# Performance work log

Hardware: AMD Instinct MI355X
Metric: run time of the kernel (lower is better)

Reference implementation:

```python
import jax, jax.numpy as jnp
import numpy as np

D_MODEL = 1024
D_INNER = 1024          # expand=1
NQK = 32
NV = 32
DSTATE = 64
DCONV = 4
CHUNK = 128
CONV_DIM = D_INNER + 2 * NQK * DSTATE          # 5120
HEADDIM = D_INNER // NV                         # 32
IN_PROJ_OUT = 2 * D_INNER + 2 * NQK * DSTATE + NV  # 6176


def setup_inputs() -> dict:
    key = jax.random.key(0)
    ks = jax.random.split(key, 6)
    B, L = 2, 8192
    u = jax.random.normal(ks[0], (B, L, D_MODEL), jnp.float32)
    W_in = jax.random.normal(ks[1], (IN_PROJ_OUT, D_MODEL), jnp.float32) * 0.02
    conv_w = jax.random.normal(ks[2], (CONV_DIM, DCONV), jnp.float32) * 0.2
    conv_b = jax.random.normal(ks[3], (CONV_DIM,), jnp.float32) * 0.02
    z_bias = jnp.zeros((D_INNER,), jnp.float32)
    D = jnp.ones((NV,), jnp.float32)
    W_out = jax.random.normal(ks[4], (D_MODEL, D_INNER), jnp.float32) * 0.02
    return {"u": u, "W_in": W_in, "conv_w": conv_w, "conv_b": conv_b,
            "z_bias": z_bias, "D": D, "W_out": W_out}


def _segsum(x):
    # x: (b,h,c,l) -> (b,h,c,l,l); entry (i,j) = sum_{j<s<=i} x_s for i>=j, masked else
    l = x.shape[-1]
    cs = jnp.cumsum(x, -1)
    seg = cs[..., :, None] - cs[..., None, :]
    mask = jnp.tril(jnp.ones((l, l), bool))
    return jnp.where(mask, seg, -1e9)


def reference(u, W_in, conv_w, conv_b, z_bias, D, W_out):
    b, L, _ = u.shape
    # in_proj and split: xBC | z | A_log
    xBCzA = u @ W_in.T
    xBC = xBCzA[..., :CONV_DIM]
    z = xBCzA[..., CONV_DIM:CONV_DIM + D_INNER]
    A_log = xBCzA[..., CONV_DIM + D_INNER:]          # (b,L,NV)
    # causal depthwise conv1d, identity activation
    xp = jnp.pad(xBC, ((0, 0), (DCONV - 1, 0), (0, 0)))
    xBC = sum(conv_w[:, k] * xp[:, k:k + L, :] for k in range(DCONV)) + conv_b
    # split x, B, C and reshape to heads
    x = xBC[..., :D_INNER].reshape(b, L, NV, HEADDIM)
    Bm = xBC[..., D_INNER:D_INNER + NQK * DSTATE].reshape(b, L, NQK, DSTATE)
    Cm = xBC[..., D_INNER + NQK * DSTATE:].reshape(b, L, NQK, DSTATE)
    # dt = softplus(A_log); A = -1 per head; kernel uses (x/dt) and multiplies dt back in
    dt = jax.nn.softplus(A_log)                      # (b,L,h)
    x_sc = x / dt[..., None]
    Xdt = x_sc * dt[..., None]
    Adt = -dt
    # chunked SSD (mamba_chunk_scan_combined math)
    nc = L // CHUNK
    Ac = Adt.reshape(b, nc, CHUNK, NV).transpose(0, 3, 1, 2)   # (b,h,c,l)
    A_cum = jnp.cumsum(Ac, -1)
    Lmat = jnp.exp(_segsum(Ac))                                # (b,h,c,l,l)
    Bc = Bm.reshape(b, nc, CHUNK, NQK, DSTATE)
    Cc = Cm.reshape(b, nc, CHUNK, NQK, DSTATE)
    Xc = Xdt.reshape(b, nc, CHUNK, NV, HEADDIM)
    # intra-chunk (diagonal block) output
    Y_diag = jnp.einsum('bclhn,bcshn,bhcls,bcshp->bclhp', Cc, Bc, Lmat, Xc)
    # per-chunk final states
    decay_states = jnp.exp(A_cum[..., -1:] - A_cum)            # (b,h,c,l)
    states = jnp.einsum('bclhn,bhcl,bclhp->bchpn', Bc, decay_states, Xc)
    dc = jnp.exp(A_cum[..., -1])                               # (b,h,c)
    st = jnp.moveaxis(states, 1, 0)                            # (c,b,h,p,n)
    dcs = jnp.moveaxis(dc, 2, 0)                               # (c,b,h)

    def step(S, inp):
        s_c, d_c = inp
        prev = S
        S = S * d_c[..., None, None] + s_c
        return S, prev

    S0 = jnp.zeros((b, NV, HEADDIM, DSTATE), Xdt.dtype)
    _, prevs = jax.lax.scan(step, S0, (st, dcs))               # (c,b,h,p,n)
    prevs = jnp.moveaxis(prevs, 0, 1)                          # (b,c,h,p,n)
    # inter-chunk (off-diagonal) contribution
    Y_off = jnp.einsum('bclhn,bchpn,bhcl->bclhp', Cc, prevs, jnp.exp(A_cum))
    y = (Y_diag + Y_off).reshape(b, L, NV, HEADDIM)
    # skip connection uses the UNscaled x (per torch code)
    y = y + D[None, None, :, None] * x
    y = y.reshape(b, L, D_INNER)
    # gated output projection
    return (y * jax.nn.silu(z + z_bias)) @ W_out.T
```

## Files before the change

kernel.cpp:

```cpp
#include <hip/hip_runtime.h>

typedef unsigned short u16;
typedef unsigned int   u32;
typedef __bf16  bf16x8 __attribute__((ext_vector_type(8)));
typedef float   f32x4  __attribute__((ext_vector_type(4)));
typedef unsigned int u32x4 __attribute__((ext_vector_type(4)));
typedef unsigned int u32x2 __attribute__((ext_vector_type(2)));

__device__ __forceinline__ float bf2f(u16 h){ return __uint_as_float(((u32)h)<<16); }
__device__ __forceinline__ u16 f2bf(float f){
  u32 u = __float_as_uint(f);
  u += 0x7FFFu + ((u>>16)&1u);
  return (u16)(u>>16);
}
__device__ __forceinline__ f32x4 mfma16(bf16x8 a, bf16x8 b, f32x4 c){
  return __builtin_amdgcn_mfma_f32_16x16x32_bf16(a,b,c,0,0,0);
}

__global__ __launch_bounds__(256) void cvt_kernel(const float* __restrict__ in,
                                                  u16* __restrict__ out, int n4){
  int i = blockIdx.x*256 + threadIdx.x;
  if (i < n4){
    float4 v = ((const float4*)in)[i];
    u32 p0 = (u32)f2bf(v.x) | ((u32)f2bf(v.y)<<16);
    u32 p1 = (u32)f2bf(v.z) | ((u32)f2bf(v.w)<<16);
    u32x2 pv = {p0, p1};
    *(u32x2*)(out + (size_t)i*4) = pv;
  }
}

__global__ __launch_bounds__(256) void dt_kernel(const float* __restrict__ u,
                                                 const float* __restrict__ Win,
                                                 float* __restrict__ dtb){
  __shared__ float us[8][1028];
  const int tid = threadIdx.x;
  const size_t t0 = (size_t)blockIdx.x*8;
  for (int i=tid; i<2048; i+=256){
    int row = i>>8, col = (i&255)*4;
    *(float4*)&us[row][col] = *(const float4*)(u + (t0+row)*1024 + col);
  }
  __syncthreads();
  const int tok = tid & 7, h = tid >> 3;
  const float* wp = Win + (size_t)(6144+h)*1024;
  float s0=0.f,s1=0.f,s2=0.f,s3=0.f;
  for (int k=0;k<1024;k+=4){
    float4 a  = *(const float4*)&us[tok][k];
    float4 wv = *(const float4*)&wp[k];
    s0 += a.x*wv.x; s1 += a.y*wv.y; s2 += a.z*wv.z; s3 += a.w*wv.w;
  }
  float s = (s0+s1)+(s2+s3);
  dtb[(t0+tok)*32 + h] = (s > 15.f) ? s : log1pf(expf(s));
}

__global__ __launch_bounds__(256,2) void gemm_in(const float* __restrict__ A,
                                                 const u16* __restrict__ Bw,
                                                 u16* __restrict__ out0,
                                                 u16* __restrict__ out1,
                                                 const float* __restrict__ zb){
  __shared__ u16 As[128*40];
  __shared__ u16 Bs[128*40];
  const int tid  = threadIdx.x;
  const int lane = tid & 63;
  const int w = tid >> 6, wm = w >> 1, wn = w & 1;
  const int quad = lane >> 4, l15 = lane & 15;
  const size_t m0 = (size_t)blockIdx.y*128, n0 = (size_t)blockIdx.x*128;

  f32x4 acc[4][4];
  #pragma unroll
  for (int i=0;i<4;i++)
    #pragma unroll
    for (int j=0;j<4;j++){ f32x4 z = {0.f,0.f,0.f,0.f}; acc[i][j] = z; }

  const int srow = tid >> 2;
  const int scol = (tid & 3) * 8;

  for (int k0 = 0; k0 < 1024; k0 += 32){
    __syncthreads();
    #pragma unroll
    for (int p=0;p<2;p++){
      int row = srow + p*64;
      const float* ap = A + (m0+row)*1024 + k0 + scol;
      float4 a0 = *(const float4*)ap;
      float4 a1 = *(const float4*)(ap+4);
      u32 w0 = (u32)f2bf(a0.x) | ((u32)f2bf(a0.y)<<16);
      u32 w1 = (u32)f2bf(a0.z) | ((u32)f2bf(a0.w)<<16);
      u32 w2 = (u32)f2bf(a1.x) | ((u32)f2bf(a1.y)<<16);
      u32 w3 = (u32)f2bf(a1.z) | ((u32)f2bf(a1.w)<<16);
      u32x4 va = {w0,w1,w2,w3};
      *(u32x4*)&As[row*40 + scol] = va;
      u32x4 vb = *(const u32x4*)(Bw + (n0+row)*1024 + k0 + scol);
      *(u32x4*)&Bs[row*40 + scol] = vb;
    }
    __syncthreads();
    bf16x8 av[4], bv[4];
    #pragma unroll
    for (int mi=0;mi<4;mi++) av[mi] = *(const bf16x8*)&As[(wm*64+mi*16+l15)*40 + quad*8];
    #pragma unroll
    for (int ni=0;ni<4;ni++) bv[ni] = *(const bf16x8*)&Bs[(wn*64+ni*16+l15)*40 + quad*8];
    #pragma unroll
    for (int mi=0;mi<4;mi++)
      #pragma unroll
      for (int ni=0;ni<4;ni++)
        acc[mi][ni] = mfma16(av[mi], bv[ni], acc[mi][ni]);
  }

  #pragma unroll
  for (int mi=0;mi<4;mi++){
    #pragma unroll
    for (int ni=0;ni<4;ni++){
      #pragma unroll
      for (int r=0;r<4;r++){
        size_t row = m0 + wm*64 + mi*16 + quad*4 + r;
        int    col = (int)n0 + wn*64 + ni*16 + l15;
        float v = acc[mi][ni][r];
        if (col < 5120){
          out0[row*5120 + col] = f2bf(v);
        } else {
          int ch = col - 5120;
          float z = v + zb[ch];
          float sg = z / (1.f + __expf(-z));
          out1[row*1024 + ch] = f2bf(sg);
        }
      }
    }
  }
}

__global__ __launch_bounds__(256,2) void gemm_out(const u16* __restrict__ A,
                                                  const u16* __restrict__ Bw,
                                                  float* __restrict__ out0){
  __shared__ u16 As[128*40];
  __shared__ u16 Bs[128*40];
  const int tid  = threadIdx.x;
  const int lane = tid & 63;
  const int w = tid >> 6, wm = w >> 1, wn = w & 1;
  const int quad = lane >> 4, l15 = lane & 15;
  const size_t m0 = (size_t)blockIdx.y*128, n0 = (size_t)blockIdx.x*128;

  f32x4 acc[4][4];
  #pragma unroll
  for (int i=0;i<4;i++)
    #pragma unroll
    for (int j=0;j<4;j++){ f32x4 z = {0.f,0.f,0.f,0.f}; acc[i][j] = z; }

  const int srow = tid >> 2;
  const int scol = (tid & 3) * 8;

  for (int k0 = 0; k0 < 1024; k0 += 32){
    __syncthreads();
    #pragma unroll
    for (int p=0;p<2;p++){
      int row = srow + p*64;
      u32x4 va = *(const u32x4*)(A  + (m0+row)*1024 + k0 + scol);
      u32x4 vb = *(const u32x4*)(Bw + (n0+row)*1024 + k0 + scol);
      *(u32x4*)&As[row*40 + scol] = va;
      *(u32x4*)&Bs[row*40 + scol] = vb;
    }
    __syncthreads();
    bf16x8 av[4], bv[4];
    #pragma unroll
    for (int mi=0;mi<4;mi++) av[mi] = *(const bf16x8*)&As[(wm*64+mi*16+l15)*40 + quad*8];
    #pragma unroll
    for (int ni=0;ni<4;ni++) bv[ni] = *(const bf16x8*)&Bs[(wn*64+ni*16+l15)*40 + quad*8];
    #pragma unroll
    for (int mi=0;mi<4;mi++)
      #pragma unroll
      for (int ni=0;ni<4;ni++)
        acc[mi][ni] = mfma16(av[mi], bv[ni], acc[mi][ni]);
  }

  #pragma unroll
  for (int mi=0;mi<4;mi++)
    #pragma unroll
    for (int ni=0;ni<4;ni++)
      #pragma unroll
      for (int r=0;r<4;r++){
        size_t row = m0 + wm*64 + mi*16 + quad*4 + r;
        int    col = (int)n0 + wn*64 + ni*16 + l15;
        out0[row*1024 + col] = acc[mi][ni][r];
      }
}

__global__ __launch_bounds__(256) void conv_kernel(const u16* __restrict__ xraw,
                                                   const float* __restrict__ cw,
                                                   const float* __restrict__ cb,
                                                   u16* __restrict__ xconv){
  const int c  = blockIdx.x*256 + threadIdx.x;
  const int t0 = blockIdx.y*8;
  const float w0=cw[c*4+0], w1=cw[c*4+1], w2=cw[c*4+2], w3=cw[c*4+3], bias=cb[c];
  const size_t base = (size_t)c;
  float h0 = (t0>=3) ? bf2f(xraw[base + (size_t)(t0-3)*5120]) : 0.f;
  float h1 = (t0>=2) ? bf2f(xraw[base + (size_t)(t0-2)*5120]) : 0.f;
  float h2 = (t0>=1) ? bf2f(xraw[base + (size_t)(t0-1)*5120]) : 0.f;
  #pragma unroll
  for (int i=0;i<8;i++){
    float x = bf2f(xraw[base + (size_t)(t0+i)*5120]);
    float o = w0*h0 + w1*h1 + w2*h2 + w3*x + bias;
    xconv[base + (size_t)(t0+i)*5120] = f2bf(o);
    h0=h1; h1=h2; h2=x;
  }
}

__global__ __launch_bounds__(256,1) void chunk1_kernel(const u16* __restrict__ xconv,
                                                       const float* __restrict__ dtb,
                                                       const float* __restrict__ Dvec,
                                                       float* __restrict__ ypart,
                                                       float* __restrict__ states,
                                                       float* __restrict__ dcb){
  __shared__ u16 Ps[128*136];
  __shared__ u16 XT[32*136];
  __shared__ u16 BT[64*136];
  __shared__ float Acum[128];
  __shared__ float decay[128];

  const int tid = threadIdx.x;
  const int lane = tid & 63;
  const int w = tid >> 6, quad = lane >> 4, l15 = lane & 15;
  const int blk = blockIdx.x;
  const int h = blk & 31, c = blk >> 5;
  const size_t tok0 = (size_t)c*128;
  const size_t xbase = tok0 * 5120;

  float mdt = 0.f;
  if (tid < 128) mdt = -dtb[(tok0 + tid)*32 + h];

  #pragma unroll
  for (int p=0;p<2;p++){
    int idx = p*256 + tid;
    int row = idx >> 2, col = (idx & 3)*8;
    u32x4 v = *(const u32x4*)(xconv + xbase + (size_t)row*5120 + h*32 + col);
    const u16* pv = (const u16*)&v;
    #pragma unroll
    for (int j=0;j<8;j++) XT[(col+j)*136 + row] = pv[j];
  }
  #pragma unroll
  for (int p=0;p<4;p++){
    int idx = p*256 + tid;
    int row = idx >> 3, col = (idx & 7)*8;
    u32x4 v = *(const u32x4*)(xconv + xbase + (size_t)row*5120 + 1024 + h*64 + col);
    const u16* pv = (const u16*)&v;
    #pragma unroll
    for (int j=0;j<8;j++) BT[(col+j)*136 + row] = pv[j];
  }
  if (tid < 128) Acum[tid] = mdt;
  __syncthreads();
  float run = mdt;
  for (int off=1; off<128; off<<=1){
    float add = 0.f;
    if (tid < 128 && tid >= off) add = Acum[tid-off];
    __syncthreads();
    if (tid < 128){ run += add; Acum[tid] = run; }
    __syncthreads();
  }
  float Alast = Acum[127];
  if (tid < 128) decay[tid] = __expf(Alast - Acum[tid]);
  if (tid == 0)  dcb[blk] = __expf(Alast);

  const int wm = w >> 1, wn = w & 1;
  f32x4 g[4][4];
  #pragma unroll
  for (int i=0;i<4;i++)
    #pragma unroll
    for (int j=0;j<4;j++){ f32x4 z = {0.f,0.f,0.f,0.f}; g[i][j] = z; }
  #pragma unroll
  for (int kk=0; kk<2; kk++){
    bf16x8 av[4], bv[4];
    #pragma unroll
    for (int mi=0;mi<4;mi++){
      int row = wm*64 + mi*16 + l15;
      av[mi] = *(const bf16x8*)(xconv + xbase + (size_t)row*5120 + 3072 + h*64 + kk*32 + quad*8);
    }
    #pragma unroll
    for (int ni=0;ni<4;ni++){
      int row = wn*64 + ni*16 + l15;
      bv[ni] = *(const bf16x8*)(xconv + xbase + (size_t)row*5120 + 1024 + h*64 + kk*32 + quad*8);
    }
    #pragma unroll
    for (int mi=0;mi<4;mi++)
      #pragma unroll
      for (int ni=0;ni<4;ni++)
        g[mi][ni] = mfma16(av[mi], bv[ni], g[mi][ni]);
  }
  #pragma unroll
  for (int mi=0;mi<4;mi++){
    int rowb = wm*64 + mi*16 + quad*4;
    #pragma unroll
    for (int ni=0;ni<4;ni++){
      int col = wn*64 + ni*16 + l15;
      float ac = Acum[col];
      #pragma unroll
      for (int r=0;r<4;r++){
        int row = rowb + r;
        float val = 0.f;
        if (col <= row) val = g[mi][ni][r] * __expf(Acum[row] - ac);
        Ps[row*136 + col] = f2bf(val);
      }
    }
  }
  __syncthreads();

  f32x4 yd[2][2];
  #pragma unroll
  for (int i=0;i<2;i++)
    #pragma unroll
    for (int j=0;j<2;j++){ f32x4 z = {0.f,0.f,0.f,0.f}; yd[i][j] = z; }
  #pragma unroll
  for (int kk=0;kk<4;kk++){
    bf16x8 av[2], bv[2];
    #pragma unroll
    for (int mi=0;mi<2;mi++) av[mi] = *(const bf16x8*)&Ps[(w*32+mi*16+l15)*136 + kk*32 + quad*8];
    #pragma unroll
    for (int ni=0;ni<2;ni++) bv[ni] = *(const bf16x8*)&XT[(ni*16+l15)*136 + kk*32 + quad*8];
    #pragma unroll
    for (int mi=0;mi<2;mi++)
      #pragma unroll
      for (int ni=0;ni<2;ni++)
        yd[mi][ni] = mfma16(av[mi], bv[ni], yd[mi][ni]);
  }
  float Dh = Dvec[h];
  #pragma unroll
  for (int mi=0;mi<2;mi++)
    #pragma unroll
    for (int ni=0;ni<2;ni++)
      #pragma unroll
      for (int r=0;r<4;r++){
        int row = w*32 + mi*16 + quad*4 + r;
        int col = ni*16 + l15;
        float xval = bf2f(XT[col*136 + row]);
        ypart[(tok0+row)*1024 + h*32 + col] = yd[mi][ni][r] + Dh*xval;
      }

  const int wm2 = w >> 1, wn2 = w & 1;
  f32x4 st[2];
  { f32x4 z = {0.f,0.f,0.f,0.f}; st[0]=z; st[1]=z; }
  #pragma unroll
  for (int kk=0;kk<4;kk++){
    bf16x8 av;
    {
      u32x4 xv = *(const u32x4*)&XT[(wm2*16+l15)*136 + kk*32 + quad*8];
      const u16* xp = (const u16*)&xv;
      #pragma unroll
      for (int j=0;j<8;j++) ((__bf16*)&av)[j] = (__bf16)(bf2f(xp[j]) * decay[kk*32 + quad*8 + j]);
    }
    bf16x8 bv[2];
    #pragma unroll
    for (int ni=0;ni<2;ni++) bv[ni] = *(const bf16x8*)&BT[(wn2*32+ni*16+l15)*136 + kk*32 + quad*8];
    #pragma unroll
    for (int ni=0;ni<2;ni++) st[ni] = mfma16(av, bv[ni], st[ni]);
  }
  size_t sbase = (size_t)blk * 2048;
  #pragma unroll
  for (int ni=0;ni<2;ni++)
    #pragma unroll
    for (int r=0;r<4;r++){
      int row = wm2*16 + quad*4 + r;
      int col = wn2*32 + ni*16 + l15;
      states[sbase + row*64 + col] = st[ni][r];
    }
}

__global__ __launch_bounds__(256) void scan_kernel(float* __restrict__ states,
                                                   const float* __restrict__ dcb){
  const int h = blockIdx.x >> 3;
  const int part = blockIdx.x & 7;
  const int pn = part*256 + threadIdx.x;
  float S = 0.f;
  for (int c=0;c<64;c++){
    size_t idx = ((size_t)(c*32 + h))*2048 + pn;
    float stv = states[idx];
    float d = dcb[c*32 + h];
    states[idx] = S;
    S = S*d + stv;
  }
}

__global__ __launch_bounds__(256,1) void chunk3_kernel(const u16* __restrict__ xconv,
                                                       const float* __restrict__ dtb,
                                                       const float* __restrict__ prevs,
                                                       const float* __restrict__ ypart,
                                                       const u16* __restrict__ gate,
                                                       u16* __restrict__ yg){
  __shared__ u16 Pv[32*72];
  __shared__ float Acum[128];
  const int tid = threadIdx.x;
  const int lane = tid & 63;
  const int w = tid >> 6, quad = lane >> 4, l15 = lane & 15;
  const int blk = blockIdx.x;
  const int h = blk & 31, c = blk >> 5;
  const size_t tok0 = (size_t)c*128;
  const size_t xbase = tok0 * 5120;

  float mdt = 0.f;
  if (tid < 128) mdt = -dtb[(tok0 + tid)*32 + h];
  size_t sbase = (size_t)blk * 2048;
  #pragma unroll
  for (int p=0;p<8;p++){
    int i = p*256 + tid;
    int pp = i >> 6, nn = i & 63;
    Pv[pp*72 + nn] = f2bf(prevs[sbase + i]);
  }
  if (tid < 128) Acum[tid] = mdt;
  __syncthreads();
  float run = mdt;
  for (int off=1; off<128; off<<=1){
    float add = 0.f;
    if (tid < 128 && tid >= off) add = Acum[tid-off];
    __syncthreads();
    if (tid < 128){ run += add; Acum[tid] = run; }
    __syncthreads();
  }

  f32x4 yo[2][2];
  #pragma unroll
  for (int i=0;i<2;i++)
    #pragma unroll
    for (int j=0;j<2;j++){ f32x4 z = {0.f,0.f,0.f,0.f}; yo[i][j] = z; }
  #pragma unroll
  for (int kk=0;kk<2;kk++){
    bf16x8 av[2], bv[2];
    #pragma unroll
    for (int mi=0;mi<2;mi++){
      int row = w*32 + mi*16 + l15;
      av[mi] = *(const bf16x8*)(xconv + xbase + (size_t)row*5120 + 3072 + h*64 + kk*32 + quad*8);
    }
    #pragma unroll
    for (int ni=0;ni<2;ni++) bv[ni] = *(const bf16x8*)&Pv[(ni*16+l15)*72 + kk*32 + quad*8];
    #pragma unroll
    for (int mi=0;mi<2;mi++)
      #pragma unroll
      for (int ni=0;ni<2;ni++)
        yo[mi][ni] = mfma16(av[mi], bv[ni], yo[mi][ni]);
  }
  #pragma unroll
  for (int mi=0;mi<2;mi++)
    #pragma unroll
    for (int ni=0;ni<2;ni++)
      #pragma unroll
      for (int r=0;r<4;r++){
        int row = w*32 + mi*16 + quad*4 + r;
        int col = ni*16 + l15;
        size_t gi = (tok0+row)*1024 + h*32 + col;
        float val = (ypart[gi] + __expf(Acum[row]) * yo[mi][ni][r]) * bf2f(gate[gi]);
        yg[gi] = f2bf(val);
      }
}

extern "C" void kernel_launch(void* const* d_in, const int* in_sizes, int n_in,
                              void* d_out, int out_size, void* d_ws, size_t ws_size,
                              hipStream_t stream){
  (void)out_size; (void)ws_size;
  static const int want[7] = {16777216, 6324224, 20480, 5120, 1024, 32, 1048576};
  const void* src[7] = {nullptr,nullptr,nullptr,nullptr,nullptr,nullptr,nullptr};
  if (n_in >= 7){
    for (int i=0;i<7;i++)
      for (int j=0;j<n_in;j++)
        if (in_sizes[j] == want[i]){ src[i] = d_in[j]; break; }
  }
  bool ok = true;
  for (int i=0;i<7;i++) if (!src[i]) ok = false;
  if (!ok) for (int i=0;i<7;i++) src[i] = d_in[i];
  const float* u      = (const float*)src[0];
  const float* W_in   = (const float*)src[1];
  const float* conv_w = (const float*)src[2];
  const float* conv_b = (const float*)src[3];
  const float* z_bias = (const float*)src[4];
  const float* Dvec   = (const float*)src[5];
  const float* W_out  = (const float*)src[6];
  float* out = (float*)d_out;

  char* p = (char*)d_ws;
  u16* wi_bf   = (u16*)p;   p += (size_t)6144*1024*2;
  u16* wo_bf   = (u16*)p;   p += (size_t)1024*1024*2;
  float* dtb   = (float*)p; p += (size_t)16384*32*4;
  u16* yg      = (u16*)p;   p += (size_t)16384*1024*2;
  float* dcb   = (float*)p; p += (size_t)4096*4;
  u16* gate    = (u16*)p;   p += (size_t)8192*1024*2;
  char* xbcA   = p;         p += (size_t)8192*5120*2;
  u16* xconv   = (u16*)p;   p += (size_t)8192*5120*2;

  u16*   xbc_raw = (u16*)xbcA;
  float* ypart   = (float*)xbcA;
  float* states  = (float*)(xbcA + (size_t)8192*1024*4);

  cvt_kernel<<<6144, 256, 0, stream>>>(W_in,  wi_bf, 6144*1024/4);
  cvt_kernel<<<1024, 256, 0, stream>>>(W_out, wo_bf, 1024*1024/4);
  dt_kernel<<<2048, 256, 0, stream>>>(u, W_in, dtb);

  for (int b = 0; b < 2; b++){
    const float* u_b   = u   + (size_t)b*8192*1024;
    float*       dtb_b = dtb + (size_t)b*8192*32;
    float*       dcb_b = dcb + (size_t)b*2048;
    u16*         yg_b  = yg  + (size_t)b*8192*1024;
    gemm_in<<<dim3(48,64), 256, 0, stream>>>(u_b, wi_bf, xbc_raw, gate, z_bias);
    conv_kernel<<<dim3(20,1024), 256, 0, stream>>>(xbc_raw, conv_w, conv_b, xconv);
    chunk1_kernel<<<2048, 256, 0, stream>>>(xconv, dtb_b, Dvec, ypart, states, dcb_b);
    scan_kernel<<<256, 256, 0, stream>>>(states, dcb_b);
    chunk3_kernel<<<2048, 256, 0, stream>>>(xconv, dtb_b, states, ypart, gate, yg_b);
  }
  gemm_out<<<dim3(8,128), 256, 0, stream>>>(yg, wo_bf, out);
}
```

Measured before the change: 848.5 us.

## Use direct global-to-LDS loads in GEMMs and pre-convert u to bf16

Adds a pass that converts the fp32 input u to bf16 before the batch loop. Both GEMMs now stage tiles with global_load_lds 16-byte transfers straight into unpadded LDS, replacing the register round-trip and the in-loop fp32-to-bf16 conversion. gemm_out moves inside the per-batch loop so the yg buffer can be halved. The cost is an extra conversion pass and unpadded LDS rows (stride 32), which may cause bank conflicts on the MFMA fragment reads.

After: 791.7 us. 1.07x faster.

```diff
diff --git a/kernel.cpp b/kernel.cpp
--- a/kernel.cpp
+++ b/kernel.cpp
@@ -15,6 +15,10 @@
 }
 __device__ __forceinline__ f32x4 mfma16(bf16x8 a, bf16x8 b, f32x4 c){
   return __builtin_amdgcn_mfma_f32_16x16x32_bf16(a,b,c,0,0,0);
+}
+__device__ __forceinline__ void ld16_lds(const u16* g, u16* l){
+  __builtin_amdgcn_global_load_lds((const __attribute__((address_space(1))) u32*)g,
+                                   (__attribute__((address_space(3))) u32*)l, 16, 0, 0);
 }
 
 __global__ __launch_bounds__(256) void cvt_kernel(const float* __restrict__ in,
@@ -52,13 +56,13 @@
   dtb[(t0+tok)*32 + h] = (s > 15.f) ? s : log1pf(expf(s));
 }
 
-__global__ __launch_bounds__(256,2) void gemm_in(const float* __restrict__ A,
+__global__ __launch_bounds__(256,2) void gemm_in(const u16* __restrict__ A,
                                                  const u16* __restrict__ Bw,
                                                  u16* __restrict__ out0,
                                                  u16* __restrict__ out1,
                                                  const float* __restrict__ zb){
-  __shared__ u16 As[128*40];
-  __shared__ u16 Bs[128*40];
+  __shared__ u16 As[128*32];
+  __shared__ u16 Bs[128*32];
   const int tid  = threadIdx.x;
   const int lane = tid & 63;
   const int w = tid >> 6, wm = w >> 1, wn = w & 1;
@@ -71,32 +75,26 @@
     #pragma unroll
     for (int j=0;j<4;j++){ f32x4 z = {0.f,0.f,0.f,0.f}; acc[i][j] = z; }
 
-  const int srow = tid >> 2;
-  const int scol = (tid & 3) * 8;
+  const int srow = w*16 + (lane>>2);
+  const int scol = (lane&3)*8;
+  const u16* gA = A  + (m0+srow)*1024 + scol;
+  const u16* gB = Bw + (n0+srow)*1024 + scol;
+  u16* lA = As + w*512;
+  u16* lB = Bs + w*512;
 
   for (int k0 = 0; k0 < 1024; k0 += 32){
     __syncthreads();
-    #pragma unroll
-    for (int p=0;p<2;p++){
-      int row = srow + p*64;
-      const float* ap = A + (m0+row)*1024 + k0 + scol;
-      float4 a0 = *(const float4*)ap;
-      float4 a1 = *(const float4*)(ap+4);
-      u32 w0 = (u32)f2bf(a0.x) | ((u32)f2bf(a0.y)<<16);
-      u32 w1 = (u32)f2bf(a0.z) | ((u32)f2bf(a0.w)<<16);
-      u32 w2 = (u32)f2bf(a1.x) | ((u32)f2bf(a1.y)<<16);
-      u32 w3 = (u32)f2bf(a1.z) | ((u32)f2bf(a1.w)<<16);
-      u32x4 va = {w0,w1,w2,w3};
-      *(u32x4*)&As[row*40 + scol] = va;
-      u32x4 vb = *(const u32x4*)(Bw + (n0+row)*1024 + k0 + scol);
-      *(u32x4*)&Bs[row*40 + scol] = vb;
-    }
+    ld16_lds(gA,          lA);
+    ld16_lds(gA + 64*1024, lA + 2048);
+    ld16_lds(gB,          lB);
+    ld16_lds(gB + 64*1024, lB + 2048);
+    gA += 32; gB += 32;
     __syncthreads();
     bf16x8 av[4], bv[4];
     #pragma unroll
-    for (int mi=0;mi<4;mi++) av[mi] = *(const bf16x8*)&As[(wm*64+mi*16+l15)*40 + quad*8];
-    #pragma unroll
-    for (int ni=0;ni<4;ni++) bv[ni] = *(const bf16x8*)&Bs[(wn*64+ni*16+l15)*40 + quad*8];
+    for (int mi=0;mi<4;mi++) av[mi] = *(const bf16x8*)&As[(wm*64+mi*16+l15)*32 + quad*8];
+    #pragma unroll
+    for (int ni=0;ni<4;ni++) bv[ni] = *(const bf16x8*)&Bs[(wn*64+ni*16+l15)*32 + quad*8];
     #pragma unroll
     for (int mi=0;mi<4;mi++)
       #pragma unroll
@@ -129,8 +127,8 @@
 __global__ __launch_bounds__(256,2) void gemm_out(const u16* __restrict__ A,
                                                   const u16* __restrict__ Bw,
                                                   float* __restrict__ out0){
-  __shared__ u16 As[128*40];
-  __shared__ u16 Bs[128*40];
+  __shared__ u16 As[128*32];
+  __shared__ u16 Bs[128*32];
   const int tid  = threadIdx.x;
   const int lane = tid & 63;
   const int w = tid >> 6, wm = w >> 1, wn = w & 1;
@@ -143,25 +141,26 @@
     #pragma unroll
     for (int j=0;j<4;j++){ f32x4 z = {0.f,0.f,0.f,0.f}; acc[i][j] = z; }
 
-  const int srow = tid >> 2;
-  const int scol = (tid & 3) * 8;
+  const int srow = w*16 + (lane>>2);
+  const int scol = (lane&3)*8;
+  const u16* gA = A  + (m0+srow)*1024 + scol;
+  const u16* gB = Bw + (n0+srow)*1024 + scol;
+  u16* lA = As + w*512;
+  u16* lB = Bs + w*512;
 
   for (int k0 = 0; k0 < 1024; k0 += 32){
     __syncthreads();
-    #pragma unroll
-    for (int p=0;p<2;p++){
-      int row = srow + p*64;
-      u32x4 va = *(const u32x4*)(A  + (m0+row)*1024 + k0 + scol);
-      u32x4 vb = *(const u32x4*)(Bw + (n0+row)*1024 + k0 + scol);
-      *(u32x4*)&As[row*40 + scol] = va;
-      *(u32x4*)&Bs[row*40 + scol] = vb;
-    }
+    ld16_lds(gA,          lA);
+    ld16_lds(gA + 64*1024, lA + 2048);
+    ld16_lds(gB,          lB);
+    ld16_lds(gB + 64*1024, lB + 2048);
+    gA += 32; gB += 32;
     __syncthreads();
     bf16x8 av[4], bv[4];
     #pragma unroll
-    for (int mi=0;mi<4;mi++) av[mi] = *(const bf16x8*)&As[(wm*64+mi*16+l15)*40 + quad*8];
-    #pragma unroll
-    for (int ni=0;ni<4;ni++) bv[ni] = *(const bf16x8*)&Bs[(wn*64+ni*16+l15)*40 + quad*8];
+    for (int mi=0;mi<4;mi++) av[mi] = *(const bf16x8*)&As[(wm*64+mi*16+l15)*32 + quad*8];
+    #pragma unroll
+    for (int ni=0;ni<4;ni++) bv[ni] = *(const bf16x8*)&Bs[(wn*64+ni*16+l15)*32 + quad*8];
     #pragma unroll
     for (int mi=0;mi<4;mi++)
       #pragma unroll
@@ -471,10 +470,11 @@
   char* p = (char*)d_ws;
   u16* wi_bf   = (u16*)p;   p += (size_t)6144*1024*2;
   u16* wo_bf   = (u16*)p;   p += (size_t)1024*1024*2;
+  u16* u_bf    = (u16*)p;   p += (size_t)16384*1024*2;
   float* dtb   = (float*)p; p += (size_t)16384*32*4;
-  u16* yg      = (u16*)p;   p += (size_t)16384*1024*2;
   float* dcb   = (float*)p; p += (size_t)4096*4;
   u16* gate    = (u16*)p;   p += (size_t)8192*1024*2;
+  u16* yg      = (u16*)p;   p += (size_t)8192*1024*2;
   char* xbcA   = p;         p += (size_t)8192*5120*2;
   u16* xconv   = (u16*)p;   p += (size_t)8192*5120*2;
 
@@ -482,20 +482,21 @@
   float* ypart   = (float*)xbcA;
   float* states  = (float*)(xbcA + (size_t)8192*1024*4);
 
-  cvt_kernel<<<6144, 256, 0, stream>>>(W_in,  wi_bf, 6144*1024/4);
-  cvt_kernel<<<1024, 256, 0, stream>>>(W_out, wo_bf, 1024*1024/4);
+  cvt_kernel<<<16384, 256, 0, stream>>>(u,     u_bf,  16384*1024/4);
+  cvt_kernel<<<6144,  256, 0, stream>>>(W_in,  wi_bf, 6144*1024/4);
+  cvt_kernel<<<1024,  256, 0, stream>>>(W_out, wo_bf, 1024*1024/4);
   dt_kernel<<<2048, 256, 0, stream>>>(u, W_in, dtb);
 
   for (int b = 0; b < 2; b++){
-    const float* u_b   = u   + (size_t)b*8192*1024;
-    float*       dtb_b = dtb + (size_t)b*8192*32;
-    float*       dcb_b = dcb + (size_t)b*2048;
-    u16*         yg_b  = yg  + (size_t)b*8192*1024;
-    gemm_in<<<dim3(48,64), 256, 0, stream>>>(u_b, wi_bf, xbc_raw, gate, z_bias);
+    const u16* ub_bf = u_bf + (size_t)b*8192*1024;
+    float*     dtb_b = dtb  + (size_t)b*8192*32;
+    float*     dcb_b = dcb  + (size_t)b*2048;
+    float*     out_b = out  + (size_t)b*8192*1024;
+    gemm_in<<<dim3(48,64), 256, 0, stream>>>(ub_bf, wi_bf, xbc_raw, gate, z_bias);
     conv_kernel<<<dim3(20,1024), 256, 0, stream>>>(xbc_raw, conv_w, conv_b, xconv);
     chunk1_kernel<<<2048, 256, 0, stream>>>(xconv, dtb_b, Dvec, ypart, states, dcb_b);
     scan_kernel<<<256, 256, 0, stream>>>(states, dcb_b);
-    chunk3_kernel<<<2048, 256, 0, stream>>>(xconv, dtb_b, states, ypart, gate, yg_b);
-  }
-  gemm_out<<<dim3(8,128), 256, 0, stream>>>(yg, wo_bf, out);
-}
+    chunk3_kernel<<<2048, 256, 0, stream>>>(xconv, dtb_b, states, ypart, gate, yg);
+    gemm_out<<<dim3(8,64), 256, 0, stream>>>(yg, wo_bf, out_b);
+  }
+}
```
